# Performance work log

Hardware: AMD Instinct MI355X
Metric: run time of the kernel (lower is better)

Reference implementation:

```python
import jax, jax.numpy as jnp
import numpy as np

PAD = 1          # kernel offsets lie in [-1, 1] for kernel_size=3
COORD_MAX = 128  # coordinates quantized to [0, 128)
S = COORD_MAX + 2 * PAD  # per-dimension encoding stride (130)


def setup_inputs() -> dict:
    key = jax.random.key(0)
    B, N, D = 4, 50000, 3
    coordinates = jax.random.randint(
        jax.random.fold_in(key, 0), (B, N, D), 0, COORD_MAX, dtype=jnp.int32)
    # batch_indices[b, n] == b, matching how the torch code partitions rows
    batch_indices = jnp.broadcast_to(jnp.arange(B, dtype=jnp.int32)[:, None], (B, N))
    # 3^3 hypercube kernel offsets, lexicographic order (KernelGenerator semantics)
    r = jnp.arange(-1, 2, dtype=jnp.int32)
    kernel_offsets = jnp.stack(jnp.meshgrid(r, r, r, indexing='ij'), axis=-1).reshape(-1, 3)
    return {"coordinates": coordinates, "batch_indices": batch_indices,
            "kernel_offsets": kernel_offsets}


def reference(coordinates, batch_indices, kernel_offsets):
    """Vectorized equivalent of LocalSelfAttention.compute_kernel_mapping.

    Returns (input_idx, output_idx, rel_pos_idx, output_key_tensor, num_unique).
    The first three are [B, N, K] (the torch kernel_map flattened row-major is
    exactly zip of these), output_key_tensor is [L, D] padded with -1 beyond
    num_unique rows, with unique keys in first-occurrence (insertion) order --
    identical to the Python dict-hashing loop.
    """
    B, N, D = coordinates.shape
    K = kernel_offsets.shape[0]
    L = B * N * K

    # neighbor coords per (point, offset): [B, N, K, D]
    nb = coordinates[:, :, None, :] + kernel_offsets[None, None, :, :]

    # encode (batch_id, neighbor_coord) into a single int32 key
    enc = jnp.broadcast_to(batch_indices[:, :, None], (B, N, K)).astype(jnp.int32)
    for d in range(D):
        enc = enc * S + (nb[..., d] + PAD)  # max ~ 4*130^3 < 2^31
    keys = enc.reshape(L)

    # sort-based dedup preserving first-occurrence order
    order = jnp.argsort(keys, stable=True)              # [L]
    sk = keys[order]
    new_group = jnp.concatenate([jnp.ones((1,), bool), sk[1:] != sk[:-1]])
    gid_sorted = jnp.cumsum(new_group.astype(jnp.int32)) - 1  # group id per sorted slot
    num_unique = gid_sorted[-1] + 1

    # first flat position where each group's key occurs (empty groups -> int32 max)
    first_occ = jax.ops.segment_min(order, gid_sorted, num_segments=L)
    # insertion-order index of each group (padded groups stably rank last)
    group_rank = jnp.argsort(jnp.argsort(first_occ))

    # scatter group ids back to original flat order, then map to insertion rank
    gid = jnp.zeros((L,), jnp.int32).at[order].set(gid_sorted)
    output_idx = group_rank[gid].reshape(B, N, K).astype(jnp.int32)

    # representative encoded key per group, reordered to insertion order
    rep_key = jax.ops.segment_min(sk, gid_sorted, num_segments=L)
    enc_ord = jnp.zeros((L,), keys.dtype).at[group_rank].set(rep_key)

    # decode neighbor coordinates (drop the batch component, as torch does)
    coords_dec = []
    e = enc_ord
    for _ in range(D):
        coords_dec.append(e % S - PAD)
        e = e // S
    out_coords = jnp.stack(coords_dec[::-1], axis=-1)  # [L, D]
    valid = (jnp.arange(L) < num_unique)[:, None]
    output_key_tensor = jnp.where(valid, out_coords, -1)

    input_idx = jnp.broadcast_to(jnp.arange(N, dtype=jnp.int32)[None, :, None], (B, N, K))
    rel_pos_idx = jnp.broadcast_to(jnp.arange(K, dtype=jnp.int32)[None, None, :], (B, N, K))
    return (input_idx, output_idx, rel_pos_idx, output_key_tensor, num_unique)
```

## Files before the change

### kernel.cpp

```cpp
#include <hip/hip_runtime.h>
#include <cstdint>

#define B_   4
#define N_   50000
#define K_   27
#define P_   (B_ * N_)
#define L_   (P_ * K_)
#define S_   130
#define PL_  (S_ * S_)
#define KS_  (B_ * S_ * S_ * S_)
#define W_   (L_ / 64)
#define NBW  ((W_ + 255) / 256)
#define BIGP 0x7f7f7f7f

__global__ __launch_bounds__(256) void k_init(int4* __restrict__ T4) {
    const int n4 = KS_ / 4;
    int4 v = make_int4(BIGP, BIGP, BIGP, BIGP);
    for (int i = blockIdx.x * blockDim.x + threadIdx.x; i < n4; i += gridDim.x * blockDim.x)
        T4[i] = v;
}

__global__ __launch_bounds__(256) void k_ptab(const int* __restrict__ coords,
                                              const int* __restrict__ bidx,
                                              int* __restrict__ P1,
                                              int* __restrict__ bpt) {
    int p = blockIdx.x * blockDim.x + threadIdx.x;
    if (p >= P_) return;
    int b = bidx[p];
    int x = coords[3 * p + 0] + 1;
    int y = coords[3 * p + 1] + 1;
    int z = coords[3 * p + 2] + 1;
    int idx = ((b * S_ + x) * S_ + y) * S_ + z;
    bpt[p] = idx;
    atomicMin(&P1[idx], p << 5);
}

__global__ __launch_bounds__(512) void k_zy(const int* __restrict__ src,
                                            int* __restrict__ dst) {
    __shared__ int pl[PL_];
    __shared__ int tz[PL_];
    const int4* s4 = (const int4*)(src + (size_t)blockIdx.x * PL_);
    int4* d4       = (int4*)(dst + (size_t)blockIdx.x * PL_);
    int4* pl4      = (int4*)pl;
    for (int i = threadIdx.x; i < PL_ / 4; i += 512) pl4[i] = s4[i];
    __syncthreads();
    for (int i = threadIdx.x; i < PL_; i += 512) {
        int z = i % S_;
        int v = pl[i] + 1;
        if (z > 0)      v = min(v, pl[i - 1] + 2);
        if (z < S_ - 1) v = min(v, pl[i + 1]);
        tz[i] = v;
    }
    __syncthreads();
    for (int i = threadIdx.x; i < PL_ / 4; i += 512) {
        int4 o;
        int base = 4 * i;
        #pragma unroll
        for (int j = 0; j < 4; ++j) {
            int idx = base + j;
            int y = idx / S_;
            int v = tz[idx] + 3;
            if (y > 0)      v = min(v, tz[idx - S_] + 6);
            if (y < S_ - 1) v = min(v, tz[idx + S_]);
            ((int*)&o)[j] = v;
        }
        d4[i] = o;
    }
}

__global__ __launch_bounds__(256) void k_x(const int4* __restrict__ src,
                                           int4* __restrict__ dst) {
    const int n4 = KS_ / 4;
    int i = blockIdx.x * blockDim.x + threadIdx.x;
    if (i >= n4) return;
    int x = (i / (PL_ / 4)) % S_;
    int4 c = src[i];
    int4 v = make_int4(c.x + 9, c.y + 9, c.z + 9, c.w + 9);
    if (x > 0) {
        int4 m = src[i - PL_ / 4];
        v.x = min(v.x, m.x + 18); v.y = min(v.y, m.y + 18);
        v.z = min(v.z, m.z + 18); v.w = min(v.w, m.w + 18);
    }
    if (x < S_ - 1) {
        int4 pp = src[i + PL_ / 4];
        v.x = min(v.x, pp.x); v.y = min(v.y, pp.y);
        v.z = min(v.z, pp.z); v.w = min(v.w, pp.w);
    }
    dst[i] = v;
}

__global__ __launch_bounds__(256) void k_gather(const int* __restrict__ bpt,
                                                const int* __restrict__ M,
                                                int* __restrict__ mArr,
                                                unsigned long long* __restrict__ bitmap,
                                                int* __restrict__ out0,
                                                int* __restrict__ out2) {
    int l = blockIdx.x * blockDim.x + threadIdx.x;
    if (l >= L_) return;
    int p = l / K_;
    int k = l - p * K_;
    out0[l] = p - (p / N_) * N_;
    out2[l] = k;
    int dx = k / 9, dy = (k / 3) % 3, dz = k - (k / 3) * 3;
    int idx = bpt[p] + (dx - 1) * PL_ + (dy - 1) * S_ + (dz - 1);
    int m32 = M[idx];
    mArr[l] = m32;
    unsigned long long bal = __ballot(m32 == ((p << 5) | k));
    if ((threadIdx.x & 63) == 0) bitmap[l >> 6] = bal;
}

__global__ __launch_bounds__(256) void k_scan_words(const unsigned long long* __restrict__ bitmap,
                                                    int* __restrict__ wpre,
                                                    int* __restrict__ bsum) {
    __shared__ int sh[256];
    int w = blockIdx.x * 256 + threadIdx.x;
    int c = (w < W_) ? __popcll(bitmap[w]) : 0;
    sh[threadIdx.x] = c;
    __syncthreads();
    for (int off = 1; off < 256; off <<= 1) {
        int t = (threadIdx.x >= off) ? sh[threadIdx.x - off] : 0;
        __syncthreads();
        sh[threadIdx.x] += t;
        __syncthreads();
    }
    if (w < W_) wpre[w] = sh[threadIdx.x] - c;
    if (threadIdx.x == 255) bsum[blockIdx.x] = sh[255];
}

__global__ __launch_bounds__(512) void k_scan_block(int* __restrict__ bsum,
                                                    int* __restrict__ num_unique_out) {
    __shared__ int sh[512];
    int i = threadIdx.x;
    int v = (i < NBW) ? bsum[i] : 0;
    sh[i] = v;
    __syncthreads();
    for (int off = 1; off < 512; off <<= 1) {
        int t = (i >= off) ? sh[i - off] : 0;
        __syncthreads();
        sh[i] += t;
        __syncthreads();
    }
    if (i < NBW) bsum[i] = sh[i] - v;
    if (i == 0) num_unique_out[0] = sh[511];
}

__global__ __launch_bounds__(256) void k_finalize(const int* __restrict__ coords,
                                                  const int* __restrict__ koffs,
                                                  const unsigned long long* __restrict__ bitmap,
                                                  const int* __restrict__ wpre,
                                                  const int* __restrict__ bsum,
                                                  const int* __restrict__ numuniq,
                                                  int* __restrict__ out1,
                                                  int* __restrict__ outkey) {
    int l = blockIdx.x * blockDim.x + threadIdx.x;
    if (l >= L_) return;
    int m32 = out1[l];
    int m = (m32 >> 5) * K_ + (m32 & 31);
    int w = m >> 6;
    unsigned long long word = bitmap[w];
    unsigned long long mask = (1ull << (m & 63)) - 1ull;
    int rank = wpre[w] + bsum[w >> 8] + (int)__popcll(word & mask);
    out1[l] = rank;
    if (m == l) {
        int p = l / K_;
        int k = l - p * K_;
        outkey[3 * rank + 0] = coords[3 * p + 0] + koffs[3 * k + 0];
        outkey[3 * rank + 1] = coords[3 * p + 1] + koffs[3 * k + 1];
        outkey[3 * rank + 2] = coords[3 * p + 2] + koffs[3 * k + 2];
    }
    if (l >= numuniq[0]) {
        outkey[3 * l + 0] = -1;
        outkey[3 * l + 1] = -1;
        outkey[3 * l + 2] = -1;
    }
}

extern "C" void kernel_launch(void* const* d_in, const int* in_sizes, int n_in,
                              void* d_out, int out_size, void* d_ws, size_t ws_size,
                              hipStream_t stream) {
    const int* coords = (const int*)d_in[0];
    const int* bidx   = (const int*)d_in[1];
    const int* koffs  = (const int*)d_in[2];

    int* out      = (int*)d_out;
    int* out0     = out;
    int* out1     = out + L_;
    int* out2     = out + 2 * L_;
    int* outkey   = out + 3 * L_;
    int* numuniq  = out + 6 * L_;

    int* P1 = (int*)d_ws;
    unsigned long long* bitmap = (unsigned long long*)(P1 + KS_);
    int* wpre = (int*)(bitmap + W_);
    int* bsum = wpre + W_;
    int* bpt  = bsum + NBW;

    int* A = outkey;

    k_init       <<<2048, 256, 0, stream>>>((int4*)P1);
    k_ptab       <<<(P_ + 255) / 256, 256, 0, stream>>>(coords, bidx, P1, bpt);
    k_zy         <<<B_ * S_, 512, 0, stream>>>(P1, A);
    k_x          <<<(KS_ / 4 + 255) / 256, 256, 0, stream>>>((const int4*)A, (int4*)P1);
    k_gather     <<<(L_ + 255) / 256, 256, 0, stream>>>(bpt, P1, out1, bitmap, out0, out2);
    k_scan_words <<<NBW, 256, 0, stream>>>(bitmap, wpre, bsum);
    k_scan_block <<<1, 512, 0, stream>>>(bsum, numuniq);
    k_finalize   <<<(L_ + 255) / 256, 256, 0, stream>>>(coords, koffs, bitmap, wpre, bsum,
                                                        numuniq, out1, outkey);
}
```

Baseline: 143.8 us.

## Store min-reduced key table in 2x4x4 tiled layout for gather locality

The dense min table after the z/y/x stencil passes is rewritten in a blocked layout of 2x4x4 cells per 32-int tile, so the 27-neighbor gather touches fewer cache lines. k_zy now processes two x-planes per block and writes the tiled layout, k_x works on the tiled indices, and bpt stores packed coordinates instead of a linear index. The cost is extra index arithmetic in gather and x-pass, plus a larger padded table (65x33x33 tiles), which the unchanged k_init may not fully cover.

```diff
diff --git a/kernel.cpp b/kernel.cpp
--- a/kernel.cpp
+++ b/kernel.cpp
@@ -13,6 +13,19 @@
 #define NBW  ((W_ + 255) / 256)
 #define BIGP 0x7f7f7f7f
 
+#define TX_  65
+#define TY_  33
+#define TZ_  33
+#define SLAB (TY_ * TZ_ * 32)
+#define MT_  (B_ * TX_ * SLAB)
+#define XT4  (SLAB / 4)
+#define ZITER ((PL_ + 511) / 512)
+
+__device__ __forceinline__ int tidx(int b, int cx, int cy, int cz) {
+    int tile = ((b * TX_ + (cx >> 1)) * TY_ + (cy >> 2)) * TZ_ + (cz >> 2);
+    return (tile << 5) + ((cx & 1) << 4) + ((cy & 3) << 2) + (cz & 3);
+}
+
 __global__ __launch_bounds__(256) void k_init(int4* __restrict__ T4) {
     const int n4 = KS_ / 4;
     int4 v = make_int4(BIGP, BIGP, BIGP, BIGP);
@@ -22,7 +35,7 @@
 
 __global__ __launch_bounds__(256) void k_ptab(const int* __restrict__ coords,
                                               const int* __restrict__ bidx,
-                                              int* __restrict__ P1,
+                                              int* __restrict__ Tlin,
                                               int* __restrict__ bpt) {
     int p = blockIdx.x * blockDim.x + threadIdx.x;
     if (p >= P_) return;
@@ -30,63 +43,96 @@
     int x = coords[3 * p + 0] + 1;
     int y = coords[3 * p + 1] + 1;
     int z = coords[3 * p + 2] + 1;
-    int idx = ((b * S_ + x) * S_ + y) * S_ + z;
-    bpt[p] = idx;
-    atomicMin(&P1[idx], p << 5);
+    bpt[p] = (b << 24) | (x << 16) | (y << 8) | z;
+    atomicMin(&Tlin[((b * S_ + x) * S_ + y) * S_ + z], p << 5);
 }
 
 __global__ __launch_bounds__(512) void k_zy(const int* __restrict__ src,
-                                            int* __restrict__ dst) {
-    __shared__ int pl[PL_];
-    __shared__ int tz[PL_];
-    const int4* s4 = (const int4*)(src + (size_t)blockIdx.x * PL_);
-    int4* d4       = (int4*)(dst + (size_t)blockIdx.x * PL_);
-    int4* pl4      = (int4*)pl;
-    for (int i = threadIdx.x; i < PL_ / 4; i += 512) pl4[i] = s4[i];
+                                            int* __restrict__ dstT) {
+    __shared__ int pl0[PL_];
+    __shared__ int pl1[PL_];
+    int blk = blockIdx.x;
+    const int* in = src + (size_t)blk * (2 * PL_);
+    int* outSlab   = dstT + (size_t)blk * SLAB;
+
+    for (int i = threadIdx.x; i < 2 * PL_; i += 512) {
+        int v = in[i];
+        if (i < PL_) pl0[i] = v; else pl1[i - PL_] = v;
+    }
     __syncthreads();
-    for (int i = threadIdx.x; i < PL_; i += 512) {
-        int z = i % S_;
-        int v = pl[i] + 1;
-        if (z > 0)      v = min(v, pl[i - 1] + 2);
-        if (z < S_ - 1) v = min(v, pl[i + 1]);
-        tz[i] = v;
-    }
-    __syncthreads();
-    for (int i = threadIdx.x; i < PL_ / 4; i += 512) {
-        int4 o;
-        int base = 4 * i;
+
+    #pragma unroll 2
+    for (int q = 0; q < 2; ++q) {
+        int* pq = q ? pl1 : pl0;
+        int r[ZITER];
         #pragma unroll
-        for (int j = 0; j < 4; ++j) {
-            int idx = base + j;
-            int y = idx / S_;
-            int v = tz[idx] + 3;
-            if (y > 0)      v = min(v, tz[idx - S_] + 6);
-            if (y < S_ - 1) v = min(v, tz[idx + S_]);
-            ((int*)&o)[j] = v;
+        for (int it = 0; it < ZITER; ++it) {
+            int j = threadIdx.x + it * 512;
+            if (j < PL_) {
+                int z = j % S_;
+                int v = pq[j] + 1;
+                if (z > 0)      v = min(v, pq[j - 1] + 2);
+                if (z < S_ - 1) v = min(v, pq[j + 1]);
+                r[it] = v;
+            }
         }
-        d4[i] = o;
+        __syncthreads();
+        #pragma unroll
+        for (int it = 0; it < ZITER; ++it) {
+            int j = threadIdx.x + it * 512;
+            if (j < PL_) pq[j] = r[it];
+        }
+        __syncthreads();
+        for (int i = threadIdx.x; i < TY_ * TZ_ * 16; i += 512) {
+            int t   = i >> 4;
+            int off = i & 15;
+            int by = t / TZ_, bz = t - by * TZ_;
+            int y = by * 4 + (off >> 2), z = bz * 4 + (off & 3);
+            if (y < S_ && z < S_) {
+                int j = y * S_ + z;
+                int v = pq[j] + 3;
+                if (y > 0)      v = min(v, pq[j - S_] + 6);
+                if (y < S_ - 1) v = min(v, pq[j + S_]);
+                outSlab[(t << 5) + (q << 4) + off] = v;
+            }
+        }
+        __syncthreads();
     }
 }
 
 __global__ __launch_bounds__(256) void k_x(const int4* __restrict__ src,
                                            int4* __restrict__ dst) {
-    const int n4 = KS_ / 4;
-    int i = blockIdx.x * blockDim.x + threadIdx.x;
-    if (i >= n4) return;
-    int x = (i / (PL_ / 4)) % S_;
-    int4 c = src[i];
+    const int n4 = MT_ / 4;
+    int i4 = blockIdx.x * blockDim.x + threadIdx.x;
+    if (i4 >= n4) return;
+    int w = i4 & 7;
+    int q = w >> 2;
+    int tile = i4 >> 3;
+    int rest = tile / TZ_;
+    rest = rest / TY_;
+    int bx = rest % TX_;
+
+    int4 c = src[i4];
     int4 v = make_int4(c.x + 9, c.y + 9, c.z + 9, c.w + 9);
-    if (x > 0) {
-        int4 m = src[i - PL_ / 4];
+    if (q == 1) {
+        int4 m = src[i4 - 4];
         v.x = min(v.x, m.x + 18); v.y = min(v.y, m.y + 18);
         v.z = min(v.z, m.z + 18); v.w = min(v.w, m.w + 18);
-    }
-    if (x < S_ - 1) {
-        int4 pp = src[i + PL_ / 4];
+    } else if (bx > 0) {
+        int4 m = src[i4 - XT4 + 4];
+        v.x = min(v.x, m.x + 18); v.y = min(v.y, m.y + 18);
+        v.z = min(v.z, m.z + 18); v.w = min(v.w, m.w + 18);
+    }
+    if (q == 0) {
+        int4 pp = src[i4 + 4];
         v.x = min(v.x, pp.x); v.y = min(v.y, pp.y);
         v.z = min(v.z, pp.z); v.w = min(v.w, pp.w);
-    }
-    dst[i] = v;
+    } else if (bx < TX_ - 1) {
+        int4 pp = src[i4 + XT4 - 4];
+        v.x = min(v.x, pp.x); v.y = min(v.y, pp.y);
+        v.z = min(v.z, pp.z); v.w = min(v.w, pp.w);
+    }
+    dst[i4] = v;
 }
 
 __global__ __launch_bounds__(256) void k_gather(const int* __restrict__ bpt,
@@ -101,9 +147,11 @@
     int k = l - p * K_;
     out0[l] = p - (p / N_) * N_;
     out2[l] = k;
+    unsigned u = (unsigned)bpt[p];
+    int b = u >> 24, x = (u >> 16) & 255, y = (u >> 8) & 255, z = u & 255;
     int dx = k / 9, dy = (k / 3) % 3, dz = k - (k / 3) * 3;
-    int idx = bpt[p] + (dx - 1) * PL_ + (dy - 1) * S_ + (dz - 1);
-    int m32 = M[idx];
+    int cx = x + dx - 1, cy = y + dy - 1, cz = z + dz - 1;
+    int m32 = M[tidx(b, cx, cy, cz)];
     mArr[l] = m32;
     unsigned long long bal = __ballot(m32 == ((p << 5) | k));
     if ((threadIdx.x & 63) == 0) bitmap[l >> 6] = bal;
@@ -189,19 +237,19 @@
     int* outkey   = out + 3 * L_;
     int* numuniq  = out + 6 * L_;
 
-    int* P1 = (int*)d_ws;
-    unsigned long long* bitmap = (unsigned long long*)(P1 + KS_);
+    int* Treg = (int*)d_ws;
+    unsigned long long* bitmap = (unsigned long long*)(Treg + MT_);
     int* wpre = (int*)(bitmap + W_);
     int* bsum = wpre + W_;
     int* bpt  = bsum + NBW;
 
     int* A = outkey;
 
-    k_init       <<<2048, 256, 0, stream>>>((int4*)P1);
-    k_ptab       <<<(P_ + 255) / 256, 256, 0, stream>>>(coords, bidx, P1, bpt);
-    k_zy         <<<B_ * S_, 512, 0, stream>>>(P1, A);
-    k_x          <<<(KS_ / 4 + 255) / 256, 256, 0, stream>>>((const int4*)A, (int4*)P1);
-    k_gather     <<<(L_ + 255) / 256, 256, 0, stream>>>(bpt, P1, out1, bitmap, out0, out2);
+    k_init       <<<2048, 256, 0, stream>>>((int4*)Treg);
+    k_ptab       <<<(P_ + 255) / 256, 256, 0, stream>>>(coords, bidx, Treg, bpt);
+    k_zy         <<<B_ * TX_, 512, 0, stream>>>(Treg, A);
+    k_x          <<<(MT_ / 4 + 255) / 256, 256, 0, stream>>>((const int4*)A, (int4*)Treg);
+    k_gather     <<<(L_ + 255) / 256, 256, 0, stream>>>(bpt, Treg, out1, bitmap, out0, out2);
     k_scan_words <<<NBW, 256, 0, stream>>>(bitmap, wpre, bsum);
     k_scan_block <<<1, 512, 0, stream>>>(bsum, numuniq);
     k_finalize   <<<(L_ + 255) / 256, 256, 0, stream>>>(coords, koffs, bitmap, wpre, bsum,
```

New measurement: 183.4 us. 27.6% more time.

## Store min-table in 4x8 y-z bricked layout to localize neighbor gathers

Applied to the files above, without the earlier changes.

The zy pass now writes the per-plane table in a tiled layout of 4x8 (y,z) bricks padded to 132x136, and the x pass and gather use that layout. Point coordinates are packed into one int so the gather can compute brick addresses. The goal is to make the 27-neighbor lookups of a wavefront fall into fewer cache lines. In exchange the table grows through padding, the x pass touches more memory, and the index arithmetic in the gather gets more complex.

```diff
diff --git a/kernel.cpp b/kernel.cpp
--- a/kernel.cpp
+++ b/kernel.cpp
@@ -13,6 +13,13 @@
 #define NBW  ((W_ + 255) / 256)
 #define BIGP 0x7f7f7f7f
 
+#define TYT  33
+#define TZT  17
+#define PLT_ (TYT * TZT * 32)
+#define PLT4 (PLT_ / 4)
+#define MT2_ (B_ * S_ * PLT_)
+#define TZP  132
+
 __global__ __launch_bounds__(256) void k_init(int4* __restrict__ T4) {
     const int n4 = KS_ / 4;
     int4 v = make_int4(BIGP, BIGP, BIGP, BIGP);
@@ -22,7 +29,7 @@
 
 __global__ __launch_bounds__(256) void k_ptab(const int* __restrict__ coords,
                                               const int* __restrict__ bidx,
-                                              int* __restrict__ P1,
+                                              int* __restrict__ Tlin,
                                               int* __restrict__ bpt) {
     int p = blockIdx.x * blockDim.x + threadIdx.x;
     if (p >= P_) return;
@@ -30,63 +37,62 @@
     int x = coords[3 * p + 0] + 1;
     int y = coords[3 * p + 1] + 1;
     int z = coords[3 * p + 2] + 1;
-    int idx = ((b * S_ + x) * S_ + y) * S_ + z;
-    bpt[p] = idx;
-    atomicMin(&P1[idx], p << 5);
+    bpt[p] = (b << 24) | (x << 16) | (y << 8) | z;
+    atomicMin(&Tlin[((b * S_ + x) * S_ + y) * S_ + z], p << 5);
 }
 
 __global__ __launch_bounds__(512) void k_zy(const int* __restrict__ src,
-                                            int* __restrict__ dst) {
+                                            int* __restrict__ dstT) {
     __shared__ int pl[PL_];
-    __shared__ int tz[PL_];
-    const int4* s4 = (const int4*)(src + (size_t)blockIdx.x * PL_);
-    int4* d4       = (int4*)(dst + (size_t)blockIdx.x * PL_);
+    __shared__ int tz[TZP * S_];
+    const int* s = src + (size_t)blockIdx.x * PL_;
+    int* d       = dstT + (size_t)blockIdx.x * PLT_;
+    const int4* s4 = (const int4*)s;
     int4* pl4      = (int4*)pl;
     for (int i = threadIdx.x; i < PL_ / 4; i += 512) pl4[i] = s4[i];
     __syncthreads();
     for (int i = threadIdx.x; i < PL_; i += 512) {
-        int z = i % S_;
+        int y = i / S_, z = i - y * S_;
         int v = pl[i] + 1;
         if (z > 0)      v = min(v, pl[i - 1] + 2);
         if (z < S_ - 1) v = min(v, pl[i + 1]);
-        tz[i] = v;
-    }
-    __syncthreads();
-    for (int i = threadIdx.x; i < PL_ / 4; i += 512) {
-        int4 o;
-        int base = 4 * i;
-        #pragma unroll
-        for (int j = 0; j < 4; ++j) {
-            int idx = base + j;
-            int y = idx / S_;
-            int v = tz[idx] + 3;
-            if (y > 0)      v = min(v, tz[idx - S_] + 6);
-            if (y < S_ - 1) v = min(v, tz[idx + S_]);
-            ((int*)&o)[j] = v;
+        tz[y * TZP + z] = v;
+    }
+    __syncthreads();
+    for (int i = threadIdx.x; i < PLT_; i += 512) {
+        int t = i >> 5, off = i & 31;
+        int by = t / TZT, bz = t - by * TZT;
+        int y = by * 4 + (off >> 3), z = bz * 8 + (off & 7);
+        int v = BIGP;
+        if (y < S_ && z < S_) {
+            int j = y * TZP + z;
+            v = tz[j] + 3;
+            if (y > 0)      v = min(v, tz[j - TZP] + 6);
+            if (y < S_ - 1) v = min(v, tz[j + TZP]);
         }
-        d4[i] = o;
+        d[i] = v;
     }
 }
 
 __global__ __launch_bounds__(256) void k_x(const int4* __restrict__ src,
                                            int4* __restrict__ dst) {
-    const int n4 = KS_ / 4;
-    int i = blockIdx.x * blockDim.x + threadIdx.x;
-    if (i >= n4) return;
-    int x = (i / (PL_ / 4)) % S_;
-    int4 c = src[i];
+    const int n4 = MT2_ / 4;
+    int i4 = blockIdx.x * blockDim.x + threadIdx.x;
+    if (i4 >= n4) return;
+    int x = (i4 / PLT4) % S_;
+    int4 c = src[i4];
     int4 v = make_int4(c.x + 9, c.y + 9, c.z + 9, c.w + 9);
     if (x > 0) {
-        int4 m = src[i - PL_ / 4];
+        int4 m = src[i4 - PLT4];
         v.x = min(v.x, m.x + 18); v.y = min(v.y, m.y + 18);
         v.z = min(v.z, m.z + 18); v.w = min(v.w, m.w + 18);
     }
     if (x < S_ - 1) {
-        int4 pp = src[i + PL_ / 4];
+        int4 pp = src[i4 + PLT4];
         v.x = min(v.x, pp.x); v.y = min(v.y, pp.y);
         v.z = min(v.z, pp.z); v.w = min(v.w, pp.w);
     }
-    dst[i] = v;
+    dst[i4] = v;
 }
 
 __global__ __launch_bounds__(256) void k_gather(const int* __restrict__ bpt,
@@ -101,8 +107,13 @@
     int k = l - p * K_;
     out0[l] = p - (p / N_) * N_;
     out2[l] = k;
+    unsigned u = (unsigned)bpt[p];
+    int b = u >> 24, x = (u >> 16) & 255, y = (u >> 8) & 255, z = u & 255;
     int dx = k / 9, dy = (k / 3) % 3, dz = k - (k / 3) * 3;
-    int idx = bpt[p] + (dx - 1) * PL_ + (dy - 1) * S_ + (dz - 1);
+    int cx = x + dx - 1, cy = y + dy - 1, cz = z + dz - 1;
+    int idx = (b * S_ + cx) * PLT_
+            + (((cy >> 2) * TZT + (cz >> 3)) << 5)
+            + ((cy & 3) << 3) + (cz & 7);
     int m32 = M[idx];
     mArr[l] = m32;
     unsigned long long bal = __ballot(m32 == ((p << 5) | k));
@@ -189,19 +200,19 @@
     int* outkey   = out + 3 * L_;
     int* numuniq  = out + 6 * L_;
 
-    int* P1 = (int*)d_ws;
-    unsigned long long* bitmap = (unsigned long long*)(P1 + KS_);
+    int* Treg = (int*)d_ws;
+    unsigned long long* bitmap = (unsigned long long*)(Treg + MT2_);
     int* wpre = (int*)(bitmap + W_);
     int* bsum = wpre + W_;
     int* bpt  = bsum + NBW;
 
     int* A = outkey;
 
-    k_init       <<<2048, 256, 0, stream>>>((int4*)P1);
-    k_ptab       <<<(P_ + 255) / 256, 256, 0, stream>>>(coords, bidx, P1, bpt);
-    k_zy         <<<B_ * S_, 512, 0, stream>>>(P1, A);
-    k_x          <<<(KS_ / 4 + 255) / 256, 256, 0, stream>>>((const int4*)A, (int4*)P1);
-    k_gather     <<<(L_ + 255) / 256, 256, 0, stream>>>(bpt, P1, out1, bitmap, out0, out2);
+    k_init       <<<2048, 256, 0, stream>>>((int4*)Treg);
+    k_ptab       <<<(P_ + 255) / 256, 256, 0, stream>>>(coords, bidx, Treg, bpt);
+    k_zy         <<<B_ * S_, 512, 0, stream>>>(Treg, A);
+    k_x          <<<(MT2_ / 4 + 255) / 256, 256, 0, stream>>>((const int4*)A, (int4*)Treg);
+    k_gather     <<<(L_ + 255) / 256, 256, 0, stream>>>(bpt, Treg, out1, bitmap, out0, out2);
     k_scan_words <<<NBW, 256, 0, stream>>>(bitmap, wpre, bsum);
     k_scan_block <<<1, 512, 0, stream>>>(bsum, numuniq);
     k_finalize   <<<(L_ + 255) / 256, 256, 0, stream>>>(coords, koffs, bitmap, wpre, bsum,
```

Result: slower. 150.4 us (+4.6%).

## Switch first-occurrence bitmap to per-point 27-bit masks with point-level scan

Applied to the files above, without the earlier changes.

The gather stage now runs one thread per point: it reads all 27 neighbour slots, writes the min-labels, and builds a 27-bit first-occurrence mask, replacing the per-element ballot bitmap. The prefix scan then runs over 200K point masks instead of 64-bit words, and out0/out2 writes move into the final kernel. Output keys are decoded from packed point coordinates rather than reloading coords and kernel offsets. The per-point kernel writes 27 strided ints per thread, which may coalesce poorly.

```diff
diff --git a/kernel.cpp b/kernel.cpp
--- a/kernel.cpp
+++ b/kernel.cpp
@@ -9,9 +9,8 @@
 #define S_   130
 #define PL_  (S_ * S_)
 #define KS_  (B_ * S_ * S_ * S_)
-#define W_   (L_ / 64)
-#define NBW  ((W_ + 255) / 256)
 #define BIGP 0x7f7f7f7f
+#define NB2  ((P_ + 1023) / 1024)
 
 __global__ __launch_bounds__(256) void k_init(int4* __restrict__ T4) {
     const int n4 = KS_ / 4;
@@ -22,7 +21,7 @@
 
 __global__ __launch_bounds__(256) void k_ptab(const int* __restrict__ coords,
                                               const int* __restrict__ bidx,
-                                              int* __restrict__ P1,
+                                              int* __restrict__ Tlin,
                                               int* __restrict__ bpt) {
     int p = blockIdx.x * blockDim.x + threadIdx.x;
     if (p >= P_) return;
@@ -30,9 +29,8 @@
     int x = coords[3 * p + 0] + 1;
     int y = coords[3 * p + 1] + 1;
     int z = coords[3 * p + 2] + 1;
-    int idx = ((b * S_ + x) * S_ + y) * S_ + z;
-    bpt[p] = idx;
-    atomicMin(&P1[idx], p << 5);
+    bpt[p] = (b << 24) | (x << 16) | (y << 8) | z;
+    atomicMin(&Tlin[((b * S_ + x) * S_ + y) * S_ + z], p << 5);
 }
 
 __global__ __launch_bounds__(512) void k_zy(const int* __restrict__ src,
@@ -89,84 +87,101 @@
     dst[i] = v;
 }
 
-__global__ __launch_bounds__(256) void k_gather(const int* __restrict__ bpt,
-                                                const int* __restrict__ M,
-                                                int* __restrict__ mArr,
-                                                unsigned long long* __restrict__ bitmap,
-                                                int* __restrict__ out0,
-                                                int* __restrict__ out2) {
+__global__ __launch_bounds__(256) void k_mask(const int* __restrict__ bpt,
+                                              const int* __restrict__ M,
+                                              int* __restrict__ m27,
+                                              unsigned* __restrict__ mask) {
+    int p = blockIdx.x * blockDim.x + threadIdx.x;
+    if (p >= P_) return;
+    unsigned u = (unsigned)bpt[p];
+    int b = u >> 24, x = (u >> 16) & 255, y = (u >> 8) & 255, z = u & 255;
+    int base = ((b * S_ + x) * S_ + y) * S_ + z;
+    int t0 = p << 5;
+    unsigned msk = 0;
+    int* o = m27 + p * K_;
+    #pragma unroll
+    for (int k = 0; k < K_; ++k) {
+        const int dx = k / 9, dy = (k / 3) % 3, dz = k - (k / 3) * 3;
+        const int off = (dx - 1) * PL_ + (dy - 1) * S_ + (dz - 1);
+        int m32 = M[base + off];
+        o[k] = m32;
+        if (m32 == (t0 | k)) msk |= (1u << k);
+    }
+    mask[p] = msk;
+}
+
+__global__ __launch_bounds__(256) void k_scan1(const unsigned* __restrict__ mask,
+                                               int* __restrict__ Cl,
+                                               int* __restrict__ bsum) {
+    __shared__ int sh[256];
+    int base = blockIdx.x * 1024 + threadIdx.x * 4;
+    int c[4], s = 0;
+    #pragma unroll
+    for (int j = 0; j < 4; ++j) {
+        int p = base + j;
+        int v = (p < P_) ? __popc(mask[p]) : 0;
+        c[j] = v; s += v;
+    }
+    sh[threadIdx.x] = s;
+    __syncthreads();
+    for (int off = 1; off < 256; off <<= 1) {
+        int t = (threadIdx.x >= off) ? sh[threadIdx.x - off] : 0;
+        __syncthreads();
+        sh[threadIdx.x] += t;
+        __syncthreads();
+    }
+    int run = sh[threadIdx.x] - s;
+    #pragma unroll
+    for (int j = 0; j < 4; ++j) {
+        int p = base + j;
+        if (p < P_) Cl[p] = run;
+        run += c[j];
+    }
+    if (threadIdx.x == 255) bsum[blockIdx.x] = sh[255];
+}
+
+__global__ __launch_bounds__(256) void k_scan2(int* __restrict__ bsum,
+                                               int* __restrict__ num_unique_out) {
+    __shared__ int sh[256];
+    int i = threadIdx.x;
+    int v = (i < NB2) ? bsum[i] : 0;
+    sh[i] = v;
+    __syncthreads();
+    for (int off = 1; off < 256; off <<= 1) {
+        int t = (i >= off) ? sh[i - off] : 0;
+        __syncthreads();
+        sh[i] += t;
+        __syncthreads();
+    }
+    if (i < NB2) bsum[i] = sh[i] - v;
+    if (i == 0) num_unique_out[0] = sh[255];
+}
+
+__global__ __launch_bounds__(256) void k_final(const unsigned* __restrict__ bpt,
+                                               const unsigned* __restrict__ mask,
+                                               const int* __restrict__ Cl,
+                                               const int* __restrict__ bsum,
+                                               const int* __restrict__ numuniq,
+                                               int* __restrict__ out0,
+                                               int* __restrict__ out1,
+                                               int* __restrict__ out2,
+                                               int* __restrict__ outkey) {
     int l = blockIdx.x * blockDim.x + threadIdx.x;
     if (l >= L_) return;
     int p = l / K_;
     int k = l - p * K_;
+    int m32 = out1[l];
+    int pf = m32 >> 5, kf = m32 & 31;
+    int rank = Cl[pf] + bsum[pf >> 10] + (int)__popc(mask[pf] & ((1u << kf) - 1u));
     out0[l] = p - (p / N_) * N_;
+    out1[l] = rank;
     out2[l] = k;
-    int dx = k / 9, dy = (k / 3) % 3, dz = k - (k / 3) * 3;
-    int idx = bpt[p] + (dx - 1) * PL_ + (dy - 1) * S_ + (dz - 1);
-    int m32 = M[idx];
-    mArr[l] = m32;
-    unsigned long long bal = __ballot(m32 == ((p << 5) | k));
-    if ((threadIdx.x & 63) == 0) bitmap[l >> 6] = bal;
-}
-
-__global__ __launch_bounds__(256) void k_scan_words(const unsigned long long* __restrict__ bitmap,
-                                                    int* __restrict__ wpre,
-                                                    int* __restrict__ bsum) {
-    __shared__ int sh[256];
-    int w = blockIdx.x * 256 + threadIdx.x;
-    int c = (w < W_) ? __popcll(bitmap[w]) : 0;
-    sh[threadIdx.x] = c;
-    __syncthreads();
-    for (int off = 1; off < 256; off <<= 1) {
-        int t = (threadIdx.x >= off) ? sh[threadIdx.x - off] : 0;
-        __syncthreads();
-        sh[threadIdx.x] += t;
-        __syncthreads();
-    }
-    if (w < W_) wpre[w] = sh[threadIdx.x] - c;
-    if (threadIdx.x == 255) bsum[blockIdx.x] = sh[255];
-}
-
-__global__ __launch_bounds__(512) void k_scan_block(int* __restrict__ bsum,
-                                                    int* __restrict__ num_unique_out) {
-    __shared__ int sh[512];
-    int i = threadIdx.x;
-    int v = (i < NBW) ? bsum[i] : 0;
-    sh[i] = v;
-    __syncthreads();
-    for (int off = 1; off < 512; off <<= 1) {
-        int t = (i >= off) ? sh[i - off] : 0;
-        __syncthreads();
-        sh[i] += t;
-        __syncthreads();
-    }
-    if (i < NBW) bsum[i] = sh[i] - v;
-    if (i == 0) num_unique_out[0] = sh[511];
-}
-
-__global__ __launch_bounds__(256) void k_finalize(const int* __restrict__ coords,
-                                                  const int* __restrict__ koffs,
-                                                  const unsigned long long* __restrict__ bitmap,
-                                                  const int* __restrict__ wpre,
-                                                  const int* __restrict__ bsum,
-                                                  const int* __restrict__ numuniq,
-                                                  int* __restrict__ out1,
-                                                  int* __restrict__ outkey) {
-    int l = blockIdx.x * blockDim.x + threadIdx.x;
-    if (l >= L_) return;
-    int m32 = out1[l];
-    int m = (m32 >> 5) * K_ + (m32 & 31);
-    int w = m >> 6;
-    unsigned long long word = bitmap[w];
-    unsigned long long mask = (1ull << (m & 63)) - 1ull;
-    int rank = wpre[w] + bsum[w >> 8] + (int)__popcll(word & mask);
-    out1[l] = rank;
-    if (m == l) {
-        int p = l / K_;
-        int k = l - p * K_;
-        outkey[3 * rank + 0] = coords[3 * p + 0] + koffs[3 * k + 0];
-        outkey[3 * rank + 1] = coords[3 * p + 1] + koffs[3 * k + 1];
-        outkey[3 * rank + 2] = coords[3 * p + 2] + koffs[3 * k + 2];
+    if (m32 == ((p << 5) | k)) {
+        unsigned u = bpt[p];
+        int dx = k / 9, dy = (k / 3) % 3, dz = k - (k / 3) * 3;
+        outkey[3 * rank + 0] = (int)((u >> 16) & 255) + dx - 2;
+        outkey[3 * rank + 1] = (int)((u >> 8) & 255) + dy - 2;
+        outkey[3 * rank + 2] = (int)(u & 255) + dz - 2;
     }
     if (l >= numuniq[0]) {
         outkey[3 * l + 0] = -1;
@@ -181,6 +196,7 @@
     const int* coords = (const int*)d_in[0];
     const int* bidx   = (const int*)d_in[1];
     const int* koffs  = (const int*)d_in[2];
+    (void)koffs;
 
     int* out      = (int*)d_out;
     int* out0     = out;
@@ -189,21 +205,21 @@
     int* outkey   = out + 3 * L_;
     int* numuniq  = out + 6 * L_;
 
-    int* P1 = (int*)d_ws;
-    unsigned long long* bitmap = (unsigned long long*)(P1 + KS_);
-    int* wpre = (int*)(bitmap + W_);
-    int* bsum = wpre + W_;
-    int* bpt  = bsum + NBW;
+    int* Treg = (int*)d_ws;
+    int* bpt  = Treg + KS_;
+    unsigned* mask = (unsigned*)(bpt + P_);
+    int* Cl   = (int*)(mask + P_);
+    int* bsum = Cl + P_;
 
     int* A = outkey;
 
-    k_init       <<<2048, 256, 0, stream>>>((int4*)P1);
-    k_ptab       <<<(P_ + 255) / 256, 256, 0, stream>>>(coords, bidx, P1, bpt);
-    k_zy         <<<B_ * S_, 512, 0, stream>>>(P1, A);
-    k_x          <<<(KS_ / 4 + 255) / 256, 256, 0, stream>>>((const int4*)A, (int4*)P1);
-    k_gather     <<<(L_ + 255) / 256, 256, 0, stream>>>(bpt, P1, out1, bitmap, out0, out2);
-    k_scan_words <<<NBW, 256, 0, stream>>>(bitmap, wpre, bsum);
-    k_scan_block <<<1, 512, 0, stream>>>(bsum, numuniq);
-    k_finalize   <<<(L_ + 255) / 256, 256, 0, stream>>>(coords, koffs, bitmap, wpre, bsum,
-                                                        numuniq, out1, outkey);
-}
+    k_init  <<<2048, 256, 0, stream>>>((int4*)Treg);
+    k_ptab  <<<(P_ + 255) / 256, 256, 0, stream>>>(coords, bidx, Treg, bpt);
+    k_zy    <<<B_ * S_, 512, 0, stream>>>(Treg, A);
+    k_x     <<<(KS_ / 4 + 255) / 256, 256, 0, stream>>>((const int4*)A, (int4*)Treg);
+    k_mask  <<<(P_ + 255) / 256, 256, 0, stream>>>(bpt, Treg, out1, mask);
+    k_scan1 <<<NB2, 256, 0, stream>>>(mask, Cl, bsum);
+    k_scan2 <<<1, 256, 0, stream>>>(bsum, numuniq);
+    k_final <<<(L_ + 255) / 256, 256, 0, stream>>>((const unsigned*)bpt, mask, Cl, bsum,
+                                                   numuniq, out0, out1, out2, outkey);
+}
```

Measured after the change: 149.5 us. 4.0% more time.
